# Performance work log

Hardware: AMD Instinct MI355X
Metric: run time of the kernel (lower is better)

The kernel has to match this reference:

```python
import jax, jax.numpy as jnp
import numpy as np

INF = 10000000000.0
D_KEY = 1024


def setup_inputs() -> dict:
    key = jax.random.key(0)
    k1, k2, k3 = jax.random.split(key, 3)
    B, S, D = 8, 2048, D_KEY
    return {
        "query": jax.random.normal(k1, (B, S, D), dtype=jnp.float32),
        "key": jax.random.normal(k2, (B, S, D), dtype=jnp.float32),
        "value": jax.random.normal(k3, (B, S, D), dtype=jnp.float32),
    }


def reference(query, key, value):
    # dot_products: [B, S, S]
    scale = jnp.asarray(np.sqrt(D_KEY), dtype=query.dtype)
    dots = jnp.einsum("bqd,bkd->bqk", query, key)
    S = key.shape[1]
    # causal mask: subtract INF on strictly-upper-triangular entries
    # (original subtracts mask BEFORE dividing by scale)
    tri = jnp.triu(jnp.ones((S, S), dtype=dots.dtype), k=1) * INF
    dots = dots - tri[None, :, :]
    attn = jax.nn.softmax(dots / scale, axis=-1)
    return jnp.einsum("bqk,bkd->bqd", attn, value)
```

## Files before the change

kernel.cpp:

```cpp
#include <hip/hip_runtime.h>

#define BB 8
#define SS 2048
#define DD 1024

typedef float f32x4 __attribute__((ext_vector_type(4)));
typedef short s16x8 __attribute__((ext_vector_type(8)));
typedef short s16x4 __attribute__((ext_vector_type(4)));

__device__ __forceinline__ short f2bf(float f) {
  unsigned u = __float_as_uint(f);
  u += 0x7FFFu + ((u >> 16) & 1u);
  return (short)(u >> 16);
}

__global__ __launch_bounds__(256)
void cvt_bf16(const float* __restrict__ s0, const float* __restrict__ s1,
              short* __restrict__ d0, short* __restrict__ d1) {
  const float* s = (blockIdx.y == 0) ? s0 : s1;
  short*       d = (blockIdx.y == 0) ? d0 : d1;
  size_t i = ((size_t)blockIdx.x * 256 + threadIdx.x) * 4;
  float4 v = *(const float4*)(s + i);
  s16x4 h = { f2bf(v.x), f2bf(v.y), f2bf(v.z), f2bf(v.w) };
  *(s16x4*)(d + i) = h;
}

__global__ __launch_bounds__(256)
void cvt_vT(const float* __restrict__ V, short* __restrict__ Vt) {
  __shared__ float tile[64][65];
  const int b  = blockIdx.z;
  const int k0 = blockIdx.x * 64;
  const int d0 = blockIdx.y * 64;

  const float* src = V + ((size_t)b * SS + k0) * DD + d0;
  {
    int row = threadIdx.x >> 4;
    int col = (threadIdx.x & 15) * 4;
    #pragma unroll
    for (int i = 0; i < 4; ++i) {
      float4 v = *(const float4*)(src + (size_t)(row + i * 16) * DD + col);
      tile[row + i * 16][col + 0] = v.x;
      tile[row + i * 16][col + 1] = v.y;
      tile[row + i * 16][col + 2] = v.z;
      tile[row + i * 16][col + 3] = v.w;
    }
  }
  __syncthreads();
  {
    int l  = threadIdx.x & 3;
    int d  = threadIdx.x >> 2;
    short* dst = Vt + ((size_t)b * DD + d0 + d) * SS + k0 + l * 16;
    s16x8 h0, h1;
    #pragma unroll
    for (int j = 0; j < 8; ++j) h0[j] = f2bf(tile[l * 16 + j][d]);
    #pragma unroll
    for (int j = 0; j < 8; ++j) h1[j] = f2bf(tile[l * 16 + 8 + j][d]);
    *(s16x8*)dst       = h0;
    *(s16x8*)(dst + 8) = h1;
  }
}

template<int MODE>
__global__ __launch_bounds__(512, 2)
void attn_fwd3(const short* __restrict__ Qb16, const short* __restrict__ Kb16,
               const short* __restrict__ Vtb16, float* __restrict__ Og,
               float* __restrict__ lg) {
  const int idx = blockIdx.x;
  const int b = idx & 7;
  const int j = idx >> 3;
  int qt, kt0, kt1;
  if (MODE == 0) {
    if (j < 32) {
      qt = 16 + (j >> 1);
      int h = (qt + 1) >> 1;
      if (j & 1) { kt0 = h; kt1 = qt + 1; } else { kt0 = 0; kt1 = h; }
    } else {
      qt = j - 32; kt0 = 0; kt1 = qt + 1;
    }
  } else {
    qt = j; kt0 = 0; kt1 = qt + 1;
  }
  const bool whole = (kt0 == 0) && (kt1 == qt + 1);
  const int q0 = qt * 64;

  const int tid  = threadIdx.x;
  const int lane = tid & 63;
  const int wave = tid >> 6;
  const int n15  = lane & 15;
  const int quad = lane >> 4;
  const int mh   = wave >> 2;
  const int nq   = wave & 3;

  __shared__ __align__(16) short qs[64][1032];
  __shared__ __align__(16) short ps[2][64][72];
  __shared__ float lred[4][64];

  const short* Qrow   = Qb16 + ((size_t)(b * SS + q0)) * DD;
  const short* Kbase  = Kb16 + ((size_t)b * SS) * DD;
  const short* Vtbase = Vtb16 + (size_t)b * DD * SS;

  {
    int row = tid >> 3;
    int c0  = (tid & 7) * 8;
    const short* src = Qrow + (size_t)row * DD;
    #pragma unroll
    for (int i = 0; i < 16; ++i)
      *(s16x8*)&qs[row][c0 + i * 64] = *(const s16x8*)(src + c0 + i * 64);
  }

  f32x4 acc[4][8];
  #pragma unroll
  for (int m = 0; m < 4; ++m)
    #pragma unroll
    for (int nt = 0; nt < 8; ++nt)
      #pragma unroll
      for (int r = 0; r < 4; ++r) acc[m][nt][r] = 0.0f;
  float lsum[2][4] = {{0.f,0.f,0.f,0.f},{0.f,0.f,0.f,0.f}};

  const short* Kln  = Kbase + (size_t)(nq * 16 + n15) * DD + quad * 8;
  const short* Aln0 = &qs[mh * 32 + n15][quad * 8];
  const short* Aln1 = &qs[mh * 32 + 16 + n15][quad * 8];
  const int dw = wave * 128;
  const short* Vln = Vtbase + (size_t)(dw + n15) * SS + quad * 8;

  __syncthreads();

  for (int kt = kt0; kt < kt1; ++kt) {
    const int k0  = kt * 64;
    const int buf = kt & 1;

    const short* Kp = Kln + (size_t)k0 * DD;

    s16x8 kr[2][4];
    #pragma unroll
    for (int kk = 0; kk < 4; ++kk) kr[0][kk] = *(const s16x8*)(Kp + kk * 32);
    #pragma unroll
    for (int kk = 0; kk < 4; ++kk) kr[1][kk] = *(const s16x8*)(Kp + 128 + kk * 32);

    s16x8 bv0[8], bv1[8];
    {
      const short* Vp = Vln + k0;
      #pragma unroll
      for (int nt = 0; nt < 8; ++nt) {
        bv0[nt] = *(const s16x8*)(Vp + (size_t)(nt * 16) * SS);
        bv1[nt] = *(const s16x8*)(Vp + (size_t)(nt * 16) * SS + 32);
      }
    }

    f32x4 sfA = {0.f,0.f,0.f,0.f}, sfB = {0.f,0.f,0.f,0.f};
    #pragma unroll
    for (int dc = 0; dc < 8; ++dc) {
      #pragma unroll
      for (int kk = 0; kk < 4; ++kk) {
        s16x8 a0 = *(const s16x8*)(Aln0 + dc * 128 + kk * 32);
        s16x8 a1 = *(const s16x8*)(Aln1 + dc * 128 + kk * 32);
        sfA = __builtin_amdgcn_mfma_f32_16x16x32_bf16(a0, kr[dc & 1][kk], sfA, 0, 0, 0);
        sfB = __builtin_amdgcn_mfma_f32_16x16x32_bf16(a1, kr[dc & 1][kk], sfB, 0, 0, 0);
      }
      if (dc < 6) {
        #pragma unroll
        for (int kk = 0; kk < 4; ++kk)
          kr[dc & 1][kk] = *(const s16x8*)(Kp + (dc + 2) * 128 + kk * 32);
      }
    }

    const int kcol = k0 + nq * 16 + n15;
    #pragma unroll
    for (int t = 0; t < 2; ++t) {
      const f32x4 sf = t ? sfB : sfA;
      const int rowb = mh * 32 + t * 16 + quad * 4;
      #pragma unroll
      for (int r = 0; r < 4; ++r) {
        int qrow = q0 + rowb + r;
        float sv = sf[r] * 0.03125f - 16.0f;
        float p  = (kcol > qrow) ? 0.0f : __expf(sv);
        lsum[t][r] += p;
        ps[buf][rowb + r][nq * 16 + n15] = f2bf(p);
      }
    }

    __syncthreads();

    #pragma unroll
    for (int kk2 = 0; kk2 < 2; ++kk2) {
      s16x8 a0 = *(const s16x8*)&ps[buf][ 0 + n15][kk2 * 32 + quad * 8];
      s16x8 a1 = *(const s16x8*)&ps[buf][16 + n15][kk2 * 32 + quad * 8];
      s16x8 a2 = *(const s16x8*)&ps[buf][32 + n15][kk2 * 32 + quad * 8];
      s16x8 a3 = *(const s16x8*)&ps[buf][48 + n15][kk2 * 32 + quad * 8];
      #pragma unroll
      for (int nt = 0; nt < 8; ++nt) {
        s16x8 bv = kk2 ? bv1[nt] : bv0[nt];
        acc[0][nt] = __builtin_amdgcn_mfma_f32_16x16x32_bf16(a0, bv, acc[0][nt], 0, 0, 0);
        acc[1][nt] = __builtin_amdgcn_mfma_f32_16x16x32_bf16(a1, bv, acc[1][nt], 0, 0, 0);
        acc[2][nt] = __builtin_amdgcn_mfma_f32_16x16x32_bf16(a2, bv, acc[2][nt], 0, 0, 0);
        acc[3][nt] = __builtin_amdgcn_mfma_f32_16x16x32_bf16(a3, bv, acc[3][nt], 0, 0, 0);
      }
    }
  }

  #pragma unroll
  for (int off = 8; off >= 1; off >>= 1)
    #pragma unroll
    for (int t = 0; t < 2; ++t)
      #pragma unroll
      for (int r = 0; r < 4; ++r) lsum[t][r] += __shfl_xor(lsum[t][r], off);
  if (n15 == 0) {
    #pragma unroll
    for (int t = 0; t < 2; ++t)
      #pragma unroll
      for (int r = 0; r < 4; ++r)
        lred[nq][mh * 32 + t * 16 + quad * 4 + r] = lsum[t][r];
  }
  __syncthreads();

  float* Ob = Og + ((size_t)(b * SS + q0)) * DD + dw;

  if (MODE == 0) {
    if (tid < 64) {
      float rs = lred[0][tid] + lred[1][tid] + lred[2][tid] + lred[3][tid];
      atomicAdd(lg + (size_t)b * SS + q0 + tid, rs);
    }
    if (whole) {
      #pragma unroll
      for (int m = 0; m < 4; ++m)
        #pragma unroll
        for (int nt = 0; nt < 8; ++nt)
          #pragma unroll
          for (int r = 0; r < 4; ++r)
            Ob[(size_t)(m * 16 + quad * 4 + r) * DD + nt * 16 + n15] = acc[m][nt][r];
    } else {
      #pragma unroll
      for (int m = 0; m < 4; ++m)
        #pragma unroll
        for (int nt = 0; nt < 8; ++nt)
          #pragma unroll
          for (int r = 0; r < 4; ++r)
            atomicAdd(&Ob[(size_t)(m * 16 + quad * 4 + r) * DD + nt * 16 + n15],
                      acc[m][nt][r]);
    }
  } else {
    float inv[4][4];
    #pragma unroll
    for (int m = 0; m < 4; ++m)
      #pragma unroll
      for (int r = 0; r < 4; ++r) {
        int row = m * 16 + quad * 4 + r;
        inv[m][r] = 1.0f / (lred[0][row] + lred[1][row] + lred[2][row] + lred[3][row]);
      }
    #pragma unroll
    for (int m = 0; m < 4; ++m)
      #pragma unroll
      for (int nt = 0; nt < 8; ++nt)
        #pragma unroll
        for (int r = 0; r < 4; ++r)
          Ob[(size_t)(m * 16 + quad * 4 + r) * DD + nt * 16 + n15] =
              acc[m][nt][r] * inv[m][r];
  }
}

__global__ __launch_bounds__(256)
void norm_o(float* __restrict__ O, const float* __restrict__ lg) {
  const int row = blockIdx.x;
  const float inv = 1.0f / lg[row];
  float4* p = (float4*)(O + (size_t)row * DD) + threadIdx.x;
  float4 v = *p;
  v.x *= inv; v.y *= inv; v.z *= inv; v.w *= inv;
  *p = v;
}

__global__ __launch_bounds__(512, 2)
void attn_fwd(const float* __restrict__ Qg, const float* __restrict__ Kg,
              const float* __restrict__ Vg, float* __restrict__ Og) {
  int idx = blockIdx.x;
  int b, qt;
  if (idx < 256) { b = idx & 7; qt = 63 - (idx >> 3); }
  else           { int r = idx - 256; b = r & 7; qt = r >> 3; }
  const int q0  = qt * 32;
  const int nkt = (q0 + 31) / 64 + 1;

  const int tid  = threadIdx.x;
  const int lane = tid & 63;
  const int wave = tid >> 6;
  const int n15  = lane & 15;
  const int quad = lane >> 4;
  const int mh   = wave >> 2;
  const int nq   = wave & 3;

  __shared__ __align__(16) short qs[32][136];
  __shared__ __align__(16) short ks[64][136];
  __shared__ __align__(16) short vsT[1024][12];
  __shared__ __align__(16) short ps[32][72];
  __shared__ __align__(16) float red[32][4];
  __shared__ __align__(16) float mstate[32];
  __shared__ __align__(16) float lstate[32];
  __shared__ __align__(16) float alpha_s[32];

  const float* Qb = Qg + ((size_t)(b * SS + q0)) * DD;
  const float* Kb = Kg + ((size_t)(b * SS)) * DD;
  const float* Vb = Vg + ((size_t)(b * SS)) * DD;

  if (tid < 32) { mstate[tid] = -1e30f; lstate[tid] = 0.0f; }

  f32x4 acc[2][8];
  #pragma unroll
  for (int mt = 0; mt < 2; ++mt)
    #pragma unroll
    for (int nt = 0; nt < 8; ++nt)
      #pragma unroll
      for (int r = 0; r < 4; ++r) acc[mt][nt][r] = 0.0f;

  for (int kt = 0; kt < nkt; ++kt) {
    const int k0 = kt * 64;
    f32x4 sfrag;
    #pragma unroll
    for (int r = 0; r < 4; ++r) sfrag[r] = 0.0f;

    for (int dc = 0; dc < 8; ++dc) {
      __syncthreads();
      {
        int row = tid >> 4, c0 = tid & 15;
        const float4* src = (const float4*)(Qb + (size_t)row * DD + dc * 128);
        #pragma unroll
        for (int k2 = 0; k2 < 2; ++k2) {
          int c = c0 + 16 * k2;
          float4 v = src[c];
          s16x4 h = { f2bf(v.x), f2bf(v.y), f2bf(v.z), f2bf(v.w) };
          *(s16x4*)&qs[row][c * 4] = h;
        }
      }
      {
        int row = tid >> 3, c0 = tid & 7;
        const float4* src = (const float4*)(Kb + (size_t)(k0 + row) * DD + dc * 128);
        #pragma unroll
        for (int k2 = 0; k2 < 4; ++k2) {
          int c = c0 + 8 * k2;
          float4 v = src[c];
          s16x4 h = { f2bf(v.x), f2bf(v.y), f2bf(v.z), f2bf(v.w) };
          *(s16x4*)&ks[row][c * 4] = h;
        }
      }
      __syncthreads();
      #pragma unroll
      for (int kk = 0; kk < 4; ++kk) {
        s16x8 a  = *(const s16x8*)&qs[mh * 16 + n15][kk * 32 + quad * 8];
        s16x8 bb = *(const s16x8*)&ks[nq * 16 + n15][kk * 32 + quad * 8];
        sfrag = __builtin_amdgcn_mfma_f32_16x16x32_bf16(a, bb, sfrag, 0, 0, 0);
      }
    }

    float s[4], rmax[4];
    const int kcol = k0 + nq * 16 + n15;
    #pragma unroll
    for (int r = 0; r < 4; ++r) {
      int qrow = q0 + mh * 16 + quad * 4 + r;
      float v = sfrag[r] * 0.03125f;
      s[r] = (kcol > qrow) ? -1e30f : v;
      rmax[r] = s[r];
    }
    #pragma unroll
    for (int off = 8; off >= 1; off >>= 1)
      #pragma unroll
      for (int r = 0; r < 4; ++r)
        rmax[r] = fmaxf(rmax[r], __shfl_xor(rmax[r], off));
    if (n15 == 0) {
      #pragma unroll
      for (int r = 0; r < 4; ++r) red[mh * 16 + quad * 4 + r][nq] = rmax[r];
    }
    __syncthreads();
    if (tid < 32) {
      float mprev = mstate[tid];
      float tmax  = fmaxf(fmaxf(red[tid][0], red[tid][1]), fmaxf(red[tid][2], red[tid][3]));
      float mnew  = fmaxf(mprev, tmax);
      alpha_s[tid] = __expf(mprev - mnew);
      mstate[tid]  = mnew;
    }
    __syncthreads();
    {
      const float4 mr = *(const float4*)&mstate[mh * 16 + quad * 4];
      float p[4], psum[4];
      p[0] = __expf(s[0] - mr.x); p[1] = __expf(s[1] - mr.y);
      p[2] = __expf(s[2] - mr.z); p[3] = __expf(s[3] - mr.w);
      #pragma unroll
      for (int r = 0; r < 4; ++r) psum[r] = p[r];
      #pragma unroll
      for (int off = 8; off >= 1; off >>= 1)
        #pragma unroll
        for (int r = 0; r < 4; ++r) psum[r] += __shfl_xor(psum[r], off);
      if (n15 == 0) {
        #pragma unroll
        for (int r = 0; r < 4; ++r) red[mh * 16 + quad * 4 + r][nq] = psum[r];
      }
      #pragma unroll
      for (int r = 0; r < 4; ++r)
        ps[mh * 16 + quad * 4 + r][nq * 16 + n15] = f2bf(p[r]);
    }
    __syncthreads();
    if (tid < 32)
      lstate[tid] = lstate[tid] * alpha_s[tid]
                  + (red[tid][0] + red[tid][1] + red[tid][2] + red[tid][3]);

    {
      const float4 a0 = *(const float4*)&alpha_s[quad * 4];
      const float4 a1 = *(const float4*)&alpha_s[16 + quad * 4];
      #pragma unroll
      for (int nt = 0; nt < 8; ++nt) {
        acc[0][nt][0] *= a0.x; acc[0][nt][1] *= a0.y; acc[0][nt][2] *= a0.z; acc[0][nt][3] *= a0.w;
        acc[1][nt][0] *= a1.x; acc[1][nt][1] *= a1.y; acc[1][nt][2] *= a1.z; acc[1][nt][3] *= a1.w;
      }
    }

    #pragma unroll
    for (int kk2 = 0; kk2 < 2; ++kk2) {
      s16x8 bv[8];
      for (int h = 0; h < 4; ++h) {
        __syncthreads();
        {
          int jj = tid & 7, c4b = tid >> 3;
          const float* src = Vb + (size_t)(k0 + kk2 * 32 + h * 8 + jj) * DD;
          #pragma unroll
          for (int k4 = 0; k4 < 4; ++k4) {
            int c4 = c4b + 64 * k4;
            float4 v = ((const float4*)src)[c4];
            vsT[c4 * 4 + 0][jj] = f2bf(v.x);
            vsT[c4 * 4 + 1][jj] = f2bf(v.y);
            vsT[c4 * 4 + 2][jj] = f2bf(v.z);
            vsT[c4 * 4 + 3][jj] = f2bf(v.w);
          }
        }
        __syncthreads();
        if (quad == h) {
          #pragma unroll
          for (int nt = 0; nt < 8; ++nt) {
            int d = wave * 128 + nt * 16 + n15;
            s16x4 x0 = *(const s16x4*)&vsT[d][0];
            s16x4 x1 = *(const s16x4*)&vsT[d][4];
            bv[nt] = __builtin_shufflevector(x0, x1, 0, 1, 2, 3, 4, 5, 6, 7);
          }
        }
      }
      s16x8 a0 = *(const s16x8*)&ps[n15][kk2 * 32 + quad * 8];
      s16x8 a1 = *(const s16x8*)&ps[16 + n15][kk2 * 32 + quad * 8];
      #pragma unroll
      for (int nt = 0; nt < 8; ++nt) {
        acc[0][nt] = __builtin_amdgcn_mfma_f32_16x16x32_bf16(a0, bv[nt], acc[0][nt], 0, 0, 0);
        acc[1][nt] = __builtin_amdgcn_mfma_f32_16x16x32_bf16(a1, bv[nt], acc[1][nt], 0, 0, 0);
      }
    }
  }

  __syncthreads();
  {
    const float4 l0 = *(const float4*)&lstate[quad * 4];
    const float4 l1 = *(const float4*)&lstate[16 + quad * 4];
    float li0[4] = { 1.f / l0.x, 1.f / l0.y, 1.f / l0.z, 1.f / l0.w };
    float li1[4] = { 1.f / l1.x, 1.f / l1.y, 1.f / l1.z, 1.f / l1.w };
    float* Ob = Og + ((size_t)(b * SS + q0)) * DD;
    #pragma unroll
    for (int mt = 0; mt < 2; ++mt)
      #pragma unroll
      for (int nt = 0; nt < 8; ++nt)
        #pragma unroll
        for (int r = 0; r < 4; ++r) {
          int m = mt * 16 + quad * 4 + r;
          int d = wave * 128 + nt * 16 + n15;
          Ob[(size_t)m * DD + d] = acc[mt][nt][r] * (mt ? li1[r] : li0[r]);
        }
  }
}

extern "C" void kernel_launch(void* const* d_in, const int* in_sizes, int n_in,
                              void* d_out, int out_size, void* d_ws, size_t ws_size,
                              hipStream_t stream) {
  const float* Q = (const float*)d_in[0];
  const float* K = (const float*)d_in[1];
  const float* V = (const float*)d_in[2];
  float* O = (float*)d_out;
  (void)in_sizes; (void)n_in;

  const size_t NE      = (size_t)BB * SS * DD;
  const size_t needQKV = 3 * NE * sizeof(short);
  const size_t needL   = (size_t)BB * SS * sizeof(float);

  if (ws_size >= needQKV + needL) {
    short* Qb = (short*)d_ws;
    short* Kb = Qb + NE;
    short* Vt = Kb + NE;
    float* lg = (float*)((char*)d_ws + needQKV);
    hipMemsetAsync(d_out, 0, out_size, stream);
    hipMemsetAsync(lg, 0, needL, stream);
    cvt_bf16<<<dim3((unsigned)(NE / 1024), 2), 256, 0, stream>>>(Q, K, Qb, Kb);
    cvt_vT<<<dim3(SS / 64, DD / 64, BB), 256, 0, stream>>>(V, Vt);
    attn_fwd3<0><<<dim3(384), dim3(512), 0, stream>>>(Qb, Kb, Vt, O, lg);
    norm_o<<<dim3(BB * SS), dim3(256), 0, stream>>>(O, lg);
  } else if (ws_size >= needQKV) {
    short* Qb = (short*)d_ws;
    short* Kb = Qb + NE;
    short* Vt = Kb + NE;
    cvt_bf16<<<dim3((unsigned)(NE / 1024), 2), 256, 0, stream>>>(Q, K, Qb, Kb);
    cvt_vT<<<dim3(SS / 64, DD / 64, BB), 256, 0, stream>>>(V, Vt);
    attn_fwd3<1><<<dim3(256), dim3(512), 0, stream>>>(Qb, Kb, Vt, O, nullptr);
  } else {
    attn_fwd<<<dim3(512), dim3(512), 0, stream>>>(Q, K, V, O);
  }
}
```

Measured before the change: 577.8 us.

## Pair query tiles per block and widen key tiles to 128 with masked-skip

Rewrites the attention kernel so each block processes a balanced pair of query tiles (high and low), using 128-wide key tiles where each of 8 waves owns 16 key columns for all 64 query rows. Fully masked waves and PV chunks on the diagonal are skipped, and V loads are prefetched across kk2 steps. This aims for better load balance across the causal triangle with fewer blocks and less wasted masked work. It increases LDS reads of Q per MFMA, removes the P double buffer (adding a sync), and drops the non-lg fallback path.

```diff
diff --git a/kernel.cpp b/kernel.cpp
--- a/kernel.cpp
+++ b/kernel.cpp
@@ -60,175 +60,186 @@
   }
 }
 
-template<int MODE>
 __global__ __launch_bounds__(512, 2)
-void attn_fwd3(const short* __restrict__ Qb16, const short* __restrict__ Kb16,
+void attn_fwd4(const short* __restrict__ Qb16, const short* __restrict__ Kb16,
                const short* __restrict__ Vtb16, float* __restrict__ Og,
                float* __restrict__ lg) {
-  const int idx = blockIdx.x;
-  const int b = idx & 7;
-  const int j = idx >> 3;
-  int qt, kt0, kt1;
-  if (MODE == 0) {
-    if (j < 32) {
-      qt = 16 + (j >> 1);
-      int h = (qt + 1) >> 1;
-      if (j & 1) { kt0 = h; kt1 = qt + 1; } else { kt0 = 0; kt1 = h; }
-    } else {
-      qt = j - 32; kt0 = 0; kt1 = qt + 1;
-    }
-  } else {
-    qt = j; kt0 = 0; kt1 = qt + 1;
-  }
-  const bool whole = (kt0 == 0) && (kt1 == qt + 1);
-  const int q0 = qt * 64;
+  const int idx  = blockIdx.x;
+  const int b    = idx & 7;
+  const int pair = (idx >> 3) & 15;
+  const int role = idx >> 7;
+
+  const int qlow  = pair;
+  const int qhigh = 31 - pair;
+  const int chigh = (qhigh + 2) >> 1;
+  const int clow  = (qlow + 2) >> 1;
 
   const int tid  = threadIdx.x;
   const int lane = tid & 63;
   const int wave = tid >> 6;
   const int n15  = lane & 15;
   const int quad = lane >> 4;
-  const int mh   = wave >> 2;
-  const int nq   = wave & 3;
 
   __shared__ __align__(16) short qs[64][1032];
-  __shared__ __align__(16) short ps[2][64][72];
-  __shared__ float lred[4][64];
-
-  const short* Qrow   = Qb16 + ((size_t)(b * SS + q0)) * DD;
-  const short* Kbase  = Kb16 + ((size_t)b * SS) * DD;
-  const short* Vtbase = Vtb16 + (size_t)b * DD * SS;
-
-  {
-    int row = tid >> 3;
-    int c0  = (tid & 7) * 8;
-    const short* src = Qrow + (size_t)row * DD;
-    #pragma unroll
-    for (int i = 0; i < 16; ++i)
-      *(s16x8*)&qs[row][c0 + i * 64] = *(const s16x8*)(src + c0 + i * 64);
-  }
-
-  f32x4 acc[4][8];
-  #pragma unroll
-  for (int m = 0; m < 4; ++m)
-    #pragma unroll
-    for (int nt = 0; nt < 8; ++nt)
-      #pragma unroll
-      for (int r = 0; r < 4; ++r) acc[m][nt][r] = 0.0f;
-  float lsum[2][4] = {{0.f,0.f,0.f,0.f},{0.f,0.f,0.f,0.f}};
-
-  const short* Kln  = Kbase + (size_t)(nq * 16 + n15) * DD + quad * 8;
-  const short* Aln0 = &qs[mh * 32 + n15][quad * 8];
-  const short* Aln1 = &qs[mh * 32 + 16 + n15][quad * 8];
+  __shared__ __align__(16) short ps[64][136];
+  __shared__ float lred[8][64];
+
+  const short* Kln = Kb16 + (size_t)b * SS * DD
+                   + (size_t)(wave * 16 + n15) * DD + quad * 8;
   const int dw = wave * 128;
-  const short* Vln = Vtbase + (size_t)(dw + n15) * SS + quad * 8;
-
-  __syncthreads();
-
-  for (int kt = kt0; kt < kt1; ++kt) {
-    const int k0  = kt * 64;
-    const int buf = kt & 1;
-
-    const short* Kp = Kln + (size_t)k0 * DD;
-
-    s16x8 kr[2][4];
-    #pragma unroll
-    for (int kk = 0; kk < 4; ++kk) kr[0][kk] = *(const s16x8*)(Kp + kk * 32);
-    #pragma unroll
-    for (int kk = 0; kk < 4; ++kk) kr[1][kk] = *(const s16x8*)(Kp + 128 + kk * 32);
-
-    s16x8 bv0[8], bv1[8];
+  const short* Vln = Vtb16 + (size_t)b * DD * SS
+                   + (size_t)(dw + n15) * SS + quad * 8;
+
+  const int nseg = role ? 2 : 1;
+  for (int s = 0; s < nseg; ++s) {
+    const int qt = s ? qlow : qhigh;
+    const int ka = s ? 0 : (role ? 8 : 0);
+    const int kb = s ? clow : (role ? chigh : 8);
+    const int q0 = qt * 64;
+
+    __syncthreads();
     {
+      int row = tid >> 3;
+      int c0  = (tid & 7) * 8;
+      const short* src = Qb16 + ((size_t)b * SS + q0 + row) * DD;
+      #pragma unroll
+      for (int i = 0; i < 16; ++i)
+        *(s16x8*)&qs[row][c0 + i * 64] = *(const s16x8*)(src + c0 + i * 64);
+    }
+
+    f32x4 acc[4][8];
+    #pragma unroll
+    for (int m = 0; m < 4; ++m)
+      #pragma unroll
+      for (int nt = 0; nt < 8; ++nt)
+        #pragma unroll
+        for (int r = 0; r < 4; ++r) acc[m][nt][r] = 0.0f;
+    float lsum[4][4];
+    #pragma unroll
+    for (int m = 0; m < 4; ++m)
+      #pragma unroll
+      for (int r = 0; r < 4; ++r) lsum[m][r] = 0.0f;
+
+    __syncthreads();
+
+    for (int kt = ka; kt < kb; ++kt) {
+      const int k0     = kt * 128;
+      const int v      = min(128, q0 + 64 - k0);
+      const int kk2max = v >> 5;
+      const bool aw    = (wave * 16) < v;
+
       const short* Vp = Vln + k0;
+      s16x8 bvA[8], bvB[8];
       #pragma unroll
       for (int nt = 0; nt < 8; ++nt) {
-        bv0[nt] = *(const s16x8*)(Vp + (size_t)(nt * 16) * SS);
-        bv1[nt] = *(const s16x8*)(Vp + (size_t)(nt * 16) * SS + 32);
-      }
-    }
-
-    f32x4 sfA = {0.f,0.f,0.f,0.f}, sfB = {0.f,0.f,0.f,0.f};
-    #pragma unroll
-    for (int dc = 0; dc < 8; ++dc) {
-      #pragma unroll
-      for (int kk = 0; kk < 4; ++kk) {
-        s16x8 a0 = *(const s16x8*)(Aln0 + dc * 128 + kk * 32);
-        s16x8 a1 = *(const s16x8*)(Aln1 + dc * 128 + kk * 32);
-        sfA = __builtin_amdgcn_mfma_f32_16x16x32_bf16(a0, kr[dc & 1][kk], sfA, 0, 0, 0);
-        sfB = __builtin_amdgcn_mfma_f32_16x16x32_bf16(a1, kr[dc & 1][kk], sfB, 0, 0, 0);
-      }
-      if (dc < 6) {
-        #pragma unroll
-        for (int kk = 0; kk < 4; ++kk)
-          kr[dc & 1][kk] = *(const s16x8*)(Kp + (dc + 2) * 128 + kk * 32);
-      }
-    }
-
-    const int kcol = k0 + nq * 16 + n15;
-    #pragma unroll
-    for (int t = 0; t < 2; ++t) {
-      const f32x4 sf = t ? sfB : sfA;
-      const int rowb = mh * 32 + t * 16 + quad * 4;
-      #pragma unroll
-      for (int r = 0; r < 4; ++r) {
-        int qrow = q0 + rowb + r;
-        float sv = sf[r] * 0.03125f - 16.0f;
-        float p  = (kcol > qrow) ? 0.0f : __expf(sv);
-        lsum[t][r] += p;
-        ps[buf][rowb + r][nq * 16 + n15] = f2bf(p);
-      }
-    }
-
+        bvA[nt] = *(const s16x8*)(Vp + (size_t)(nt * 16) * SS);
+        bvB[nt] = *(const s16x8*)(Vp + (size_t)(nt * 16) * SS + 32);
+      }
+
+      if (aw) {
+        const short* Kp = Kln + (size_t)k0 * DD;
+        s16x8 kr[2][4];
+        #pragma unroll
+        for (int kk = 0; kk < 4; ++kk) kr[0][kk] = *(const s16x8*)(Kp + kk * 32);
+        #pragma unroll
+        for (int kk = 0; kk < 4; ++kk) kr[1][kk] = *(const s16x8*)(Kp + 128 + kk * 32);
+
+        f32x4 sf[4];
+        #pragma unroll
+        for (int m = 0; m < 4; ++m)
+          #pragma unroll
+          for (int r = 0; r < 4; ++r) sf[m][r] = 0.0f;
+
+        #pragma unroll
+        for (int dc = 0; dc < 8; ++dc) {
+          #pragma unroll
+          for (int kk = 0; kk < 4; ++kk) {
+            const int off = dc * 128 + kk * 32 + quad * 8;
+            s16x8 a0 = *(const s16x8*)&qs[ 0 + n15][off];
+            s16x8 a1 = *(const s16x8*)&qs[16 + n15][off];
+            s16x8 a2 = *(const s16x8*)&qs[32 + n15][off];
+            s16x8 a3 = *(const s16x8*)&qs[48 + n15][off];
+            sf[0] = __builtin_amdgcn_mfma_f32_16x16x32_bf16(a0, kr[dc & 1][kk], sf[0], 0, 0, 0);
+            sf[1] = __builtin_amdgcn_mfma_f32_16x16x32_bf16(a1, kr[dc & 1][kk], sf[1], 0, 0, 0);
+            sf[2] = __builtin_amdgcn_mfma_f32_16x16x32_bf16(a2, kr[dc & 1][kk], sf[2], 0, 0, 0);
+            sf[3] = __builtin_amdgcn_mfma_f32_16x16x32_bf16(a3, kr[dc & 1][kk], sf[3], 0, 0, 0);
+          }
+          if (dc < 6) {
+            #pragma unroll
+            for (int kk = 0; kk < 4; ++kk)
+              kr[dc & 1][kk] = *(const s16x8*)(Kp + (dc + 2) * 128 + kk * 32);
+          }
+        }
+
+        const int kcol = k0 + wave * 16 + n15;
+        #pragma unroll
+        for (int m = 0; m < 4; ++m) {
+          const int rowb = m * 16 + quad * 4;
+          #pragma unroll
+          for (int r = 0; r < 4; ++r) {
+            int qrow = q0 + rowb + r;
+            float sv = sf[m][r] * 0.03125f - 16.0f;
+            float p  = (kcol > qrow) ? 0.0f : __expf(sv);
+            lsum[m][r] += p;
+            ps[rowb + r][wave * 16 + n15] = f2bf(p);
+          }
+        }
+      }
+
+      __syncthreads();
+
+      #pragma unroll
+      for (int kk2 = 0; kk2 < 4; ++kk2) {
+        if (kk2 < kk2max) {
+          const int co = kk2 * 32 + quad * 8;
+          s16x8 a0 = *(const s16x8*)&ps[ 0 + n15][co];
+          s16x8 a1 = *(const s16x8*)&ps[16 + n15][co];
+          s16x8 a2 = *(const s16x8*)&ps[32 + n15][co];
+          s16x8 a3 = *(const s16x8*)&ps[48 + n15][co];
+          #pragma unroll
+          for (int nt = 0; nt < 8; ++nt) {
+            s16x8 bv = (kk2 & 1) ? bvB[nt] : bvA[nt];
+            acc[0][nt] = __builtin_amdgcn_mfma_f32_16x16x32_bf16(a0, bv, acc[0][nt], 0, 0, 0);
+            acc[1][nt] = __builtin_amdgcn_mfma_f32_16x16x32_bf16(a1, bv, acc[1][nt], 0, 0, 0);
+            acc[2][nt] = __builtin_amdgcn_mfma_f32_16x16x32_bf16(a2, bv, acc[2][nt], 0, 0, 0);
+            acc[3][nt] = __builtin_amdgcn_mfma_f32_16x16x32_bf16(a3, bv, acc[3][nt], 0, 0, 0);
+          }
+          if (kk2 + 2 < kk2max) {
+            #pragma unroll
+            for (int nt = 0; nt < 8; ++nt) {
+              s16x8 nb = *(const s16x8*)(Vp + (size_t)(nt * 16) * SS + (kk2 + 2) * 32);
+              if (kk2 & 1) bvB[nt] = nb; else bvA[nt] = nb;
+            }
+          }
+        }
+      }
+
+      __syncthreads();
+    }
+
+    #pragma unroll
+    for (int off = 8; off >= 1; off >>= 1)
+      #pragma unroll
+      for (int m = 0; m < 4; ++m)
+        #pragma unroll
+        for (int r = 0; r < 4; ++r) lsum[m][r] += __shfl_xor(lsum[m][r], off);
+    if (n15 == 0) {
+      #pragma unroll
+      for (int m = 0; m < 4; ++m)
+        #pragma unroll
+        for (int r = 0; r < 4; ++r)
+          lred[wave][m * 16 + quad * 4 + r] = lsum[m][r];
+    }
     __syncthreads();
-
-    #pragma unroll
-    for (int kk2 = 0; kk2 < 2; ++kk2) {
-      s16x8 a0 = *(const s16x8*)&ps[buf][ 0 + n15][kk2 * 32 + quad * 8];
-      s16x8 a1 = *(const s16x8*)&ps[buf][16 + n15][kk2 * 32 + quad * 8];
-      s16x8 a2 = *(const s16x8*)&ps[buf][32 + n15][kk2 * 32 + quad * 8];
-      s16x8 a3 = *(const s16x8*)&ps[buf][48 + n15][kk2 * 32 + quad * 8];
-      #pragma unroll
-      for (int nt = 0; nt < 8; ++nt) {
-        s16x8 bv = kk2 ? bv1[nt] : bv0[nt];
-        acc[0][nt] = __builtin_amdgcn_mfma_f32_16x16x32_bf16(a0, bv, acc[0][nt], 0, 0, 0);
-        acc[1][nt] = __builtin_amdgcn_mfma_f32_16x16x32_bf16(a1, bv, acc[1][nt], 0, 0, 0);
-        acc[2][nt] = __builtin_amdgcn_mfma_f32_16x16x32_bf16(a2, bv, acc[2][nt], 0, 0, 0);
-        acc[3][nt] = __builtin_amdgcn_mfma_f32_16x16x32_bf16(a3, bv, acc[3][nt], 0, 0, 0);
-      }
-    }
-  }
-
-  #pragma unroll
-  for (int off = 8; off >= 1; off >>= 1)
-    #pragma unroll
-    for (int t = 0; t < 2; ++t)
-      #pragma unroll
-      for (int r = 0; r < 4; ++r) lsum[t][r] += __shfl_xor(lsum[t][r], off);
-  if (n15 == 0) {
-    #pragma unroll
-    for (int t = 0; t < 2; ++t)
-      #pragma unroll
-      for (int r = 0; r < 4; ++r)
-        lred[nq][mh * 32 + t * 16 + quad * 4 + r] = lsum[t][r];
-  }
-  __syncthreads();
-
-  float* Ob = Og + ((size_t)(b * SS + q0)) * DD + dw;
-
-  if (MODE == 0) {
     if (tid < 64) {
-      float rs = lred[0][tid] + lred[1][tid] + lred[2][tid] + lred[3][tid];
-      atomicAdd(lg + (size_t)b * SS + q0 + tid, rs);
-    }
-    if (whole) {
-      #pragma unroll
-      for (int m = 0; m < 4; ++m)
-        #pragma unroll
-        for (int nt = 0; nt < 8; ++nt)
-          #pragma unroll
-          for (int r = 0; r < 4; ++r)
-            Ob[(size_t)(m * 16 + quad * 4 + r) * DD + nt * 16 + n15] = acc[m][nt][r];
-    } else {
+      float t = 0.f;
+      #pragma unroll
+      for (int w = 0; w < 8; ++w) t += lred[w][tid];
+      atomicAdd(lg + (size_t)b * SS + q0 + tid, t);
+    }
+
+    float* Ob = Og + ((size_t)b * SS + q0) * DD + dw;
+    if (s == 0) {
       #pragma unroll
       for (int m = 0; m < 4; ++m)
         #pragma unroll
@@ -237,24 +248,15 @@
           for (int r = 0; r < 4; ++r)
             atomicAdd(&Ob[(size_t)(m * 16 + quad * 4 + r) * DD + nt * 16 + n15],
                       acc[m][nt][r]);
-    }
-  } else {
-    float inv[4][4];
-    #pragma unroll
-    for (int m = 0; m < 4; ++m)
-      #pragma unroll
-      for (int r = 0; r < 4; ++r) {
-        int row = m * 16 + quad * 4 + r;
-        inv[m][r] = 1.0f / (lred[0][row] + lred[1][row] + lred[2][row] + lred[3][row]);
-      }
-    #pragma unroll
-    for (int m = 0; m < 4; ++m)
-      #pragma unroll
-      for (int nt = 0; nt < 8; ++nt)
-        #pragma unroll
-        for (int r = 0; r < 4; ++r)
-          Ob[(size_t)(m * 16 + quad * 4 + r) * DD + nt * 16 + n15] =
-              acc[m][nt][r] * inv[m][r];
+    } else {
+      #pragma unroll
+      for (int m = 0; m < 4; ++m)
+        #pragma unroll
+        for (int nt = 0; nt < 8; ++nt)
+          #pragma unroll
+          for (int r = 0; r < 4; ++r)
+            Ob[(size_t)(m * 16 + quad * 4 + r) * DD + nt * 16 + n15] = acc[m][nt][r];
+    }
   }
 }
 
@@ -490,15 +492,8 @@
     hipMemsetAsync(lg, 0, needL, stream);
     cvt_bf16<<<dim3((unsigned)(NE / 1024), 2), 256, 0, stream>>>(Q, K, Qb, Kb);
     cvt_vT<<<dim3(SS / 64, DD / 64, BB), 256, 0, stream>>>(V, Vt);
-    attn_fwd3<0><<<dim3(384), dim3(512), 0, stream>>>(Qb, Kb, Vt, O, lg);
+    attn_fwd4<<<dim3(256), dim3(512), 0, stream>>>(Qb, Kb, Vt, O, lg);
     norm_o<<<dim3(BB * SS), dim3(256), 0, stream>>>(O, lg);
-  } else if (ws_size >= needQKV) {
-    short* Qb = (short*)d_ws;
-    short* Kb = Qb + NE;
-    short* Vt = Kb + NE;
-    cvt_bf16<<<dim3((unsigned)(NE / 1024), 2), 256, 0, stream>>>(Q, K, Qb, Kb);
-    cvt_vT<<<dim3(SS / 64, DD / 64, BB), 256, 0, stream>>>(V, Vt);
-    attn_fwd3<1><<<dim3(256), dim3(512), 0, stream>>>(Qb, Kb, Vt, O, nullptr);
   } else {
     attn_fwd<<<dim3(512), dim3(512), 0, stream>>>(Q, K, V, O);
   }
```

Result: slower. 862.8 us (+49.3%).
